# Kernel optimization log

Hardware: AMD Instinct MI355X
Metric: run time of the kernel (lower is better)

Reference implementation:

```python
import jax, jax.numpy as jnp
import numpy as np

B, IN, OUT, NC, S = 4096, 512, 512, 64, 1


def setup_inputs() -> dict:
    key = jax.random.key(0)
    k = jax.random.split(key, 5)
    x = jax.random.normal(k[0], (B, IN), dtype=jnp.float32)
    centers = jax.random.normal(k[1], (NC, IN), dtype=jnp.float32)
    log_sigma = jnp.zeros((NC,), dtype=jnp.float32)
    coeff_mean = jax.random.normal(k[2], (IN, OUT, NC), dtype=jnp.float32) * 0.05
    coeff_log_var = jnp.full((IN, OUT, NC), -5.0, dtype=jnp.float32)
    base_weight = jax.random.normal(k[3], (IN, OUT), dtype=jnp.float32) * 0.05
    eps = jax.random.normal(k[4], (S, IN, OUT, NC), dtype=jnp.float32)
    return {"x": x, "centers": centers, "log_sigma": log_sigma,
            "coeff_mean": coeff_mean, "coeff_log_var": coeff_log_var,
            "base_weight": base_weight, "eps": eps}


def reference(x, centers, log_sigma, coeff_mean, coeff_log_var, base_weight, eps):
    # RBF basis: (B, NC). Original repeats this along in_features, but the
    # einsum 'bin,ion->bo' with an i-constant basis equals rbf @ coeffs.sum(i).
    dist_sq = jnp.sum((x[:, None, :] - centers[None, :, :]) ** 2, axis=-1)  # (B, NC)
    sigma = jnp.exp(log_sigma)  # (NC,)
    rbf = jnp.exp(-dist_sq / (2.0 * sigma ** 2 + 1e-8))  # (B, NC)

    # Sampled variational coefficients, reparameterized.
    std = jnp.exp(0.5 * coeff_log_var)
    coeffs = coeff_mean + eps * std            # (S, IN, OUT, NC)
    c_sum = coeffs.sum(axis=1)                 # (S, OUT, NC): sum over in_features
    n_samples = eps.shape[0]
    rbf_out = jnp.einsum('bn,son->bo', rbf, c_sum) / n_samples  # mean over samples

    out = rbf_out + x @ base_weight

    # KL vs N(0, 1) prior (prior_scale = 1.0): log(var/prior_var) = coeff_log_var
    var = jnp.exp(coeff_log_var)
    kl = 0.5 * jnp.sum(var + coeff_mean ** 2 - 1.0 - coeff_log_var)
    return out, kl
```

## Files before the change

kernel.cpp:

```cpp
#include <hip/hip_runtime.h>
#include <hip/hip_bf16.h>

#define B_SZ  4096
#define IN_F  512
#define OUT_F 512
#define NC    64
#define PAIRS 32768
#define TOT   (IN_F * PAIRS)
#define KTOT  (IN_F + NC)
#define RCH   64

typedef __attribute__((ext_vector_type(8))) short bf16x8;
typedef __attribute__((ext_vector_type(4))) float f32x4;

static __device__ inline unsigned short f2bf(float f) {
    __hip_bfloat16 h = __float2bfloat16(f);
    return *(unsigned short*)&h;
}

__global__ __launch_bounds__(1024)
void k1_partial(const float* __restrict__ cm,
                const float* __restrict__ clv,
                const float* __restrict__ eps,
                float* __restrict__ part,
                float* __restrict__ klpart,
                int S) {
    int pb = blockIdx.x & 7;
    int rc = blockIdx.x >> 3;
    int p4 = pb * 4096 + threadIdx.x * 4;
    float Sf = (float)S;
    float4 s = {0.f, 0.f, 0.f, 0.f};
    float klp = 0.f;

#pragma unroll 4
    for (int ii = 0; ii < 8; ++ii) {
        size_t idx = (size_t)(rc * 8 + ii) * PAIRS + p4;
        float4 m  = *(const float4*)(cm  + idx);
        float4 lv = *(const float4*)(clv + idx);
        float4 es = *(const float4*)(eps + idx);
        for (int si = 1; si < S; ++si) {
            float4 e2 = *(const float4*)(eps + (size_t)si * TOT + idx);
            es.x += e2.x; es.y += e2.y; es.z += e2.z; es.w += e2.w;
        }
        float e1x = __expf(0.5f * lv.x);
        float e1y = __expf(0.5f * lv.y);
        float e1z = __expf(0.5f * lv.z);
        float e1w = __expf(0.5f * lv.w);
        s.x += Sf * m.x + es.x * e1x;
        s.y += Sf * m.y + es.y * e1y;
        s.z += Sf * m.z + es.z * e1z;
        s.w += Sf * m.w + es.w * e1w;
        klp += (e1x*e1x + m.x*m.x - 1.f - lv.x);
        klp += (e1y*e1y + m.y*m.y - 1.f - lv.y);
        klp += (e1z*e1z + m.z*m.z - 1.f - lv.z);
        klp += (e1w*e1w + m.w*m.w - 1.f - lv.w);
    }

    *(float4*)(part + (size_t)rc * PAIRS + p4) = s;

    for (int off = 32; off; off >>= 1)
        klp += __shfl_down(klp, off, 64);
    __shared__ float wsum[16];
    if ((threadIdx.x & 63) == 0) wsum[threadIdx.x >> 6] = klp;
    __syncthreads();
    if (threadIdx.x == 0) {
        float t = 0.f;
#pragma unroll
        for (int i = 0; i < 16; ++i) t += wsum[i];
        klpart[blockIdx.x] = t;
    }
}

__global__ __launch_bounds__(256)
void k_mid(const float* __restrict__ part,
           const float* __restrict__ klpart,
           const float* __restrict__ bw,
           unsigned short* __restrict__ wct,
           float* __restrict__ kl_out,
           float inv_S) {
    __shared__ float tile[64 * 68];
    __shared__ float wsum[4];
    int bid = blockIdx.x, t = threadIdx.x;

    if (bid < 128) {
        int p = bid * 256 + t;
        float a = 0.f;
#pragma unroll 8
        for (int r = 0; r < RCH; ++r)
            a += part[(size_t)r * PAIRS + p];
        int o = p >> 6, n = p & 63;
        wct[(size_t)o * KTOT + IN_F + n] = f2bf(a * inv_S);
    } else if (bid < 192) {
        int bb = bid - 128;
        int bi = bb >> 3, bj = bb & 7;
        int cq = t & 15, rq = t >> 4;
#pragma unroll
        for (int rr = 0; rr < 4; ++rr) {
            int row = rq * 4 + rr;
            float4 v = *(const float4*)(bw + (size_t)(bi * 64 + row) * OUT_F + bj * 64 + cq * 4);
            *(float4*)&tile[row * 68 + cq * 4] = v;
        }
        __syncthreads();
#pragma unroll
        for (int rr = 0; rr < 4; ++rr) {
            int orow = rq * 4 + rr;
            ushort4 w;
            w.x = f2bf(tile[(cq * 4 + 0) * 68 + orow]);
            w.y = f2bf(tile[(cq * 4 + 1) * 68 + orow]);
            w.z = f2bf(tile[(cq * 4 + 2) * 68 + orow]);
            w.w = f2bf(tile[(cq * 4 + 3) * 68 + orow]);
            *(ushort4*)(wct + (size_t)(bj * 64 + orow) * KTOT + bi * 64 + cq * 4) = w;
        }
    } else {
        float v = klpart[t] + klpart[t + 256];
        for (int off = 32; off; off >>= 1)
            v += __shfl_down(v, off, 64);
        if ((t & 63) == 0) wsum[t >> 6] = v;
        __syncthreads();
        if (t == 0)
            kl_out[0] = 0.5f * (wsum[0] + wsum[1] + wsum[2] + wsum[3]);
    }
}

__global__ __launch_bounds__(512)
void k2_rbf(const float* __restrict__ x,
            const float* __restrict__ centers,
            const float* __restrict__ log_sigma,
            unsigned short* __restrict__ rbf) {
    __shared__ float red[16][8][64];
    int t = threadIdx.x;
    int n = t & 63;
    int wu = __builtin_amdgcn_readfirstlane(t >> 6);
    int b0 = blockIdx.x * 16;

    float creg[64];
#pragma unroll
    for (int q = 0; q < 16; ++q) {
        float4 v = *(const float4*)(centers + (size_t)n * IN_F + wu * 64 + q * 4);
        creg[q * 4 + 0] = v.x; creg[q * 4 + 1] = v.y;
        creg[q * 4 + 2] = v.z; creg[q * 4 + 3] = v.w;
    }

    float dacc[16];
#pragma unroll
    for (int bi = 0; bi < 16; ++bi) {
        const float* xr = x + (size_t)(b0 + bi) * IN_F + wu * 64;
        float d0 = 0.f, d1 = 0.f, d2 = 0.f, d3 = 0.f;
#pragma unroll
        for (int j = 0; j < 64; j += 4) {
            float t0 = xr[j + 0] - creg[j + 0];
            float t1 = xr[j + 1] - creg[j + 1];
            float t2 = xr[j + 2] - creg[j + 2];
            float t3 = xr[j + 3] - creg[j + 3];
            d0 = fmaf(t0, t0, d0); d1 = fmaf(t1, t1, d1);
            d2 = fmaf(t2, t2, d2); d3 = fmaf(t3, t3, d3);
        }
        dacc[bi] = (d0 + d1) + (d2 + d3);
    }

#pragma unroll
    for (int bi = 0; bi < 16; ++bi)
        red[bi][wu][n] = dacc[bi];
    __syncthreads();

#pragma unroll
    for (int pass = 0; pass < 2; ++pass) {
        int idx = pass * 512 + t;
        int bi = idx >> 6, nn = idx & 63;
        float s = 0.f;
#pragma unroll
        for (int w = 0; w < 8; ++w) s += red[bi][w][nn];
        float sg  = __expf(log_sigma[nn]);
        float inv = 1.f / (2.f * sg * sg + 1e-8f);
        rbf[(size_t)(b0 + bi) * NC + nn] = f2bf(__expf(-s * inv));
    }
}

__global__ __launch_bounds__(256)
void k3_mfma(const float* __restrict__ x,
             const unsigned short* __restrict__ rbf,
             const unsigned short* __restrict__ wct,
             float* __restrict__ out) {
    __shared__ __align__(16) unsigned short As[64 * 40];
    __shared__ __align__(16) unsigned short Bs[64 * 40];
    int t = threadIdx.x;
    int bm = blockIdx.x >> 3, bn = blockIdx.x & 7;
    int b0 = bm * 64, o0 = bn * 64;
    int r = t >> 2, ks = t & 3;
    int lane = t & 63, wv = t >> 6;
    int fm = lane & 15, kg = lane >> 4;

    f32x4 acc[4] = {{0,0,0,0},{0,0,0,0},{0,0,0,0},{0,0,0,0}};
    const int soff = r * 40 + ks * 8;
    const int aoff = (wv * 16 + fm) * 40 + kg * 8;

    for (int it = 0; it < 16; ++it) {
        int k0 = it * 32;
        float4 xa = *(const float4*)(x + (size_t)(b0 + r) * IN_F + k0 + ks * 8);
        float4 xb = *(const float4*)(x + (size_t)(b0 + r) * IN_F + k0 + ks * 8 + 4);
        ushort4 w0 = *(const ushort4*)(wct + (size_t)(o0 + r) * KTOT + k0 + ks * 8);
        ushort4 w1 = *(const ushort4*)(wct + (size_t)(o0 + r) * KTOT + k0 + ks * 8 + 4);
        __syncthreads();
        ushort4 a0 = {f2bf(xa.x), f2bf(xa.y), f2bf(xa.z), f2bf(xa.w)};
        ushort4 a1 = {f2bf(xb.x), f2bf(xb.y), f2bf(xb.z), f2bf(xb.w)};
        *(ushort4*)&As[soff]     = a0;
        *(ushort4*)&As[soff + 4] = a1;
        *(ushort4*)&Bs[soff]     = w0;
        *(ushort4*)&Bs[soff + 4] = w1;
        __syncthreads();
        bf16x8 af = *(bf16x8*)&As[aoff];
#pragma unroll
        for (int nf = 0; nf < 4; ++nf) {
            bf16x8 bfr = *(bf16x8*)&Bs[(nf * 16 + fm) * 40 + kg * 8];
            acc[nf] = __builtin_amdgcn_mfma_f32_16x16x32_bf16(af, bfr, acc[nf], 0, 0, 0);
        }
    }

    for (int it = 0; it < 2; ++it) {
        int k0 = it * 32;
        ushort4 r0 = *(const ushort4*)(rbf + (size_t)(b0 + r) * NC + k0 + ks * 8);
        ushort4 r1 = *(const ushort4*)(rbf + (size_t)(b0 + r) * NC + k0 + ks * 8 + 4);
        ushort4 w0 = *(const ushort4*)(wct + (size_t)(o0 + r) * KTOT + IN_F + k0 + ks * 8);
        ushort4 w1 = *(const ushort4*)(wct + (size_t)(o0 + r) * KTOT + IN_F + k0 + ks * 8 + 4);
        __syncthreads();
        *(ushort4*)&As[soff]     = r0;
        *(ushort4*)&As[soff + 4] = r1;
        *(ushort4*)&Bs[soff]     = w0;
        *(ushort4*)&Bs[soff + 4] = w1;
        __syncthreads();
        bf16x8 af = *(bf16x8*)&As[aoff];
#pragma unroll
        for (int nf = 0; nf < 4; ++nf) {
            bf16x8 bfr = *(bf16x8*)&Bs[(nf * 16 + fm) * 40 + kg * 8];
            acc[nf] = __builtin_amdgcn_mfma_f32_16x16x32_bf16(af, bfr, acc[nf], 0, 0, 0);
        }
    }

#pragma unroll
    for (int nf = 0; nf < 4; ++nf)
#pragma unroll
        for (int rr = 0; rr < 4; ++rr)
            out[(size_t)(b0 + wv * 16 + kg * 4 + rr) * OUT_F + o0 + nf * 16 + fm] = acc[nf][rr];
}

extern "C" void kernel_launch(void* const* d_in, const int* in_sizes, int n_in,
                              void* d_out, int out_size, void* d_ws, size_t ws_size,
                              hipStream_t stream) {
    const float* x         = (const float*)d_in[0];
    const float* centers   = (const float*)d_in[1];
    const float* log_sigma = (const float*)d_in[2];
    const float* cm        = (const float*)d_in[3];
    const float* clv       = (const float*)d_in[4];
    const float* bw        = (const float*)d_in[5];
    const float* eps       = (const float*)d_in[6];

    float* out = (float*)d_out;
    float* kl  = out + (size_t)B_SZ * OUT_F;

    float* part   = (float*)d_ws;
    float* klpart = part + (size_t)RCH * PAIRS;
    unsigned short* wct = (unsigned short*)(klpart + 512);
    unsigned short* rbf = wct + (size_t)OUT_F * KTOT;

    int S = in_sizes[6] / TOT;

    k1_partial<<<512, 1024, 0, stream>>>(cm, clv, eps, part, klpart, S);
    k_mid<<<193, 256, 0, stream>>>(part, klpart, bw, wct, kl, 1.0f / (float)S);
    k2_rbf<<<B_SZ / 16, 512, 0, stream>>>(x, centers, log_sigma, rbf);
    k3_mfma<<<(B_SZ / 64) * (OUT_F / 64), 256, 0, stream>>>(x, rbf, wct, out);
}
```

Before: 264.8 us.

## Fuse RBF kernel into mid kernel and batch loads in partial reduction

```diff
diff --git a/kernel.cpp b/kernel.cpp
--- a/kernel.cpp
+++ b/kernel.cpp
@@ -18,92 +18,155 @@
     return *(unsigned short*)&h;
 }
 
-__global__ __launch_bounds__(1024)
+__global__ __launch_bounds__(512)
 void k1_partial(const float* __restrict__ cm,
                 const float* __restrict__ clv,
                 const float* __restrict__ eps,
                 float* __restrict__ part,
                 float* __restrict__ klpart,
                 int S) {
-    int pb = blockIdx.x & 7;
-    int rc = blockIdx.x >> 3;
-    int p4 = pb * 4096 + threadIdx.x * 4;
+    int pb = blockIdx.x & 15;
+    int rc = blockIdx.x >> 4;
+    int p4 = pb * 2048 + (threadIdx.x << 2);
+    size_t base = (size_t)(rc * 8) * PAIRS + p4;
     float Sf = (float)S;
+
+    float4 M[8], LV[8], ES[8];
+#pragma unroll
+    for (int ii = 0; ii < 8; ++ii)
+        M[ii] = *(const float4*)(cm + base + (size_t)ii * PAIRS);
+#pragma unroll
+    for (int ii = 0; ii < 8; ++ii)
+        LV[ii] = *(const float4*)(clv + base + (size_t)ii * PAIRS);
+#pragma unroll
+    for (int ii = 0; ii < 8; ++ii)
+        ES[ii] = *(const float4*)(eps + base + (size_t)ii * PAIRS);
+    for (int si = 1; si < S; ++si)
+#pragma unroll
+        for (int ii = 0; ii < 8; ++ii) {
+            float4 e = *(const float4*)(eps + (size_t)si * TOT + base + (size_t)ii * PAIRS);
+            ES[ii].x += e.x; ES[ii].y += e.y; ES[ii].z += e.z; ES[ii].w += e.w;
+        }
+
     float4 s = {0.f, 0.f, 0.f, 0.f};
     float klp = 0.f;
-
-#pragma unroll 4
+#pragma unroll
     for (int ii = 0; ii < 8; ++ii) {
-        size_t idx = (size_t)(rc * 8 + ii) * PAIRS + p4;
-        float4 m  = *(const float4*)(cm  + idx);
-        float4 lv = *(const float4*)(clv + idx);
-        float4 es = *(const float4*)(eps + idx);
-        for (int si = 1; si < S; ++si) {
-            float4 e2 = *(const float4*)(eps + (size_t)si * TOT + idx);
-            es.x += e2.x; es.y += e2.y; es.z += e2.z; es.w += e2.w;
-        }
-        float e1x = __expf(0.5f * lv.x);
-        float e1y = __expf(0.5f * lv.y);
-        float e1z = __expf(0.5f * lv.z);
-        float e1w = __expf(0.5f * lv.w);
-        s.x += Sf * m.x + es.x * e1x;
-        s.y += Sf * m.y + es.y * e1y;
-        s.z += Sf * m.z + es.z * e1z;
-        s.w += Sf * m.w + es.w * e1w;
-        klp += (e1x*e1x + m.x*m.x - 1.f - lv.x);
-        klp += (e1y*e1y + m.y*m.y - 1.f - lv.y);
-        klp += (e1z*e1z + m.z*m.z - 1.f - lv.z);
-        klp += (e1w*e1w + m.w*m.w - 1.f - lv.w);
+        float e1x = __expf(0.5f * LV[ii].x);
+        float e1y = __expf(0.5f * LV[ii].y);
+        float e1z = __expf(0.5f * LV[ii].z);
+        float e1w = __expf(0.5f * LV[ii].w);
+        s.x += Sf * M[ii].x + ES[ii].x * e1x;
+        s.y += Sf * M[ii].y + ES[ii].y * e1y;
+        s.z += Sf * M[ii].z + ES[ii].z * e1z;
+        s.w += Sf * M[ii].w + ES[ii].w * e1w;
+        klp += (e1x*e1x + M[ii].x*M[ii].x - 1.f - LV[ii].x);
+        klp += (e1y*e1y + M[ii].y*M[ii].y - 1.f - LV[ii].y);
+        klp += (e1z*e1z + M[ii].z*M[ii].z - 1.f - LV[ii].z);
+        klp += (e1w*e1w + M[ii].w*M[ii].w - 1.f - LV[ii].w);
     }
 
     *(float4*)(part + (size_t)rc * PAIRS + p4) = s;
 
     for (int off = 32; off; off >>= 1)
         klp += __shfl_down(klp, off, 64);
-    __shared__ float wsum[16];
+    __shared__ float wsum[8];
     if ((threadIdx.x & 63) == 0) wsum[threadIdx.x >> 6] = klp;
     __syncthreads();
     if (threadIdx.x == 0) {
         float t = 0.f;
 #pragma unroll
-        for (int i = 0; i < 16; ++i) t += wsum[i];
+        for (int i = 0; i < 8; ++i) t += wsum[i];
         klpart[blockIdx.x] = t;
     }
 }
 
-__global__ __launch_bounds__(256)
-void k_mid(const float* __restrict__ part,
+__global__ __launch_bounds__(512)
+void k_mid(const float* __restrict__ x,
+           const float* __restrict__ centers,
+           const float* __restrict__ log_sigma,
+           const float* __restrict__ part,
            const float* __restrict__ klpart,
            const float* __restrict__ bw,
+           unsigned short* __restrict__ rbf,
            unsigned short* __restrict__ wct,
            float* __restrict__ kl_out,
            float inv_S) {
-    __shared__ float tile[64 * 68];
-    __shared__ float wsum[4];
+    __shared__ float shbuf[16 * 8 * 64];
     int bid = blockIdx.x, t = threadIdx.x;
 
-    if (bid < 128) {
-        int p = bid * 256 + t;
-        float a = 0.f;
-#pragma unroll 8
-        for (int r = 0; r < RCH; ++r)
-            a += part[(size_t)r * PAIRS + p];
+    if (bid < 256) {
+        float (*red)[8][64] = (float (*)[8][64])shbuf;
+        int n = t & 63;
+        int wu = __builtin_amdgcn_readfirstlane(t >> 6);
+        int b0 = bid * 16;
+
+        float creg[64];
+#pragma unroll
+        for (int q = 0; q < 16; ++q) {
+            float4 v = *(const float4*)(centers + (size_t)n * IN_F + wu * 64 + q * 4);
+            creg[q * 4 + 0] = v.x; creg[q * 4 + 1] = v.y;
+            creg[q * 4 + 2] = v.z; creg[q * 4 + 3] = v.w;
+        }
+
+        float dacc[16];
+#pragma unroll
+        for (int bi = 0; bi < 16; ++bi) {
+            const float* xr = x + (size_t)(b0 + bi) * IN_F + wu * 64;
+            float d0 = 0.f, d1 = 0.f, d2 = 0.f, d3 = 0.f;
+#pragma unroll
+            for (int j = 0; j < 64; j += 4) {
+                float t0 = xr[j + 0] - creg[j + 0];
+                float t1 = xr[j + 1] - creg[j + 1];
+                float t2 = xr[j + 2] - creg[j + 2];
+                float t3 = xr[j + 3] - creg[j + 3];
+                d0 = fmaf(t0, t0, d0); d1 = fmaf(t1, t1, d1);
+                d2 = fmaf(t2, t2, d2); d3 = fmaf(t3, t3, d3);
+            }
+            dacc[bi] = (d0 + d1) + (d2 + d3);
+        }
+#pragma unroll
+        for (int bi = 0; bi < 16; ++bi)
+            red[bi][wu][n] = dacc[bi];
+        __syncthreads();
+#pragma unroll
+        for (int pass = 0; pass < 2; ++pass) {
+            int idx = pass * 512 + t;
+            int bi = idx >> 6, nn = idx & 63;
+            float ssum = 0.f;
+#pragma unroll
+            for (int w = 0; w < 8; ++w) ssum += red[bi][w][nn];
+            float sg  = __expf(log_sigma[nn]);
+            float inv = 1.f / (2.f * sg * sg + 1e-8f);
+            rbf[(size_t)(b0 + bi) * NC + nn] = f2bf(__expf(-ssum * inv));
+        }
+    } else if (bid < 320) {
+        int p = (bid - 256) * 512 + t;
+        float a0 = 0.f, a1 = 0.f, a2 = 0.f, a3 = 0.f;
+#pragma unroll
+        for (int r = 0; r < RCH; r += 4) {
+            a0 += part[(size_t)(r + 0) * PAIRS + p];
+            a1 += part[(size_t)(r + 1) * PAIRS + p];
+            a2 += part[(size_t)(r + 2) * PAIRS + p];
+            a3 += part[(size_t)(r + 3) * PAIRS + p];
+        }
         int o = p >> 6, n = p & 63;
-        wct[(size_t)o * KTOT + IN_F + n] = f2bf(a * inv_S);
-    } else if (bid < 192) {
-        int bb = bid - 128;
+        wct[(size_t)o * KTOT + IN_F + n] = f2bf(((a0 + a1) + (a2 + a3)) * inv_S);
+    } else if (bid < 384) {
+        float* tile = shbuf;
+        int bb = bid - 320;
         int bi = bb >> 3, bj = bb & 7;
         int cq = t & 15, rq = t >> 4;
 #pragma unroll
-        for (int rr = 0; rr < 4; ++rr) {
-            int row = rq * 4 + rr;
+        for (int rr = 0; rr < 2; ++rr) {
+            int row = rq * 2 + rr;
             float4 v = *(const float4*)(bw + (size_t)(bi * 64 + row) * OUT_F + bj * 64 + cq * 4);
             *(float4*)&tile[row * 68 + cq * 4] = v;
         }
         __syncthreads();
 #pragma unroll
-        for (int rr = 0; rr < 4; ++rr) {
-            int orow = rq * 4 + rr;
+        for (int rr = 0; rr < 2; ++rr) {
+            int orow = rq * 2 + rr;
             ushort4 w;
             w.x = f2bf(tile[(cq * 4 + 0) * 68 + orow]);
             w.y = f2bf(tile[(cq * 4 + 1) * 68 + orow]);
@@ -112,67 +175,18 @@
             *(ushort4*)(wct + (size_t)(bj * 64 + orow) * KTOT + bi * 64 + cq * 4) = w;
         }
     } else {
-        float v = klpart[t] + klpart[t + 256];
+        float v = klpart[t] + klpart[t + 512];
         for (int off = 32; off; off >>= 1)
             v += __shfl_down(v, off, 64);
+        float* wsum = shbuf;
         if ((t & 63) == 0) wsum[t >> 6] = v;
         __syncthreads();
-        if (t == 0)
-            kl_out[0] = 0.5f * (wsum[0] + wsum[1] + wsum[2] + wsum[3]);
-    }
-}
-
-__global__ __launch_bounds__(512)
-void k2_rbf(const float* __restrict__ x,
-            const float* __restrict__ centers,
-            const float* __restrict__ log_sigma,
-            unsigned short* __restrict__ rbf) {
-    __shared__ float red[16][8][64];
-    int t = threadIdx.x;
-    int n = t & 63;
-    int wu = __builtin_amdgcn_readfirstlane(t >> 6);
-    int b0 = blockIdx.x * 16;
-
-    float creg[64];
-#pragma unroll
-    for (int q = 0; q < 16; ++q) {
-        float4 v = *(const float4*)(centers + (size_t)n * IN_F + wu * 64 + q * 4);
-        creg[q * 4 + 0] = v.x; creg[q * 4 + 1] = v.y;
-        creg[q * 4 + 2] = v.z; creg[q * 4 + 3] = v.w;
-    }
-
-    float dacc[16];
-#pragma unroll
-    for (int bi = 0; bi < 16; ++bi) {
-        const float* xr = x + (size_t)(b0 + bi) * IN_F + wu * 64;
-        float d0 = 0.f, d1 = 0.f, d2 = 0.f, d3 = 0.f;
-#pragma unroll
-        for (int j = 0; j < 64; j += 4) {
-            float t0 = xr[j + 0] - creg[j + 0];
-            float t1 = xr[j + 1] - creg[j + 1];
-            float t2 = xr[j + 2] - creg[j + 2];
-            float t3 = xr[j + 3] - creg[j + 3];
-            d0 = fmaf(t0, t0, d0); d1 = fmaf(t1, t1, d1);
-            d2 = fmaf(t2, t2, d2); d3 = fmaf(t3, t3, d3);
-        }
-        dacc[bi] = (d0 + d1) + (d2 + d3);
-    }
-
-#pragma unroll
-    for (int bi = 0; bi < 16; ++bi)
-        red[bi][wu][n] = dacc[bi];
-    __syncthreads();
-
-#pragma unroll
-    for (int pass = 0; pass < 2; ++pass) {
-        int idx = pass * 512 + t;
-        int bi = idx >> 6, nn = idx & 63;
-        float s = 0.f;
-#pragma unroll
-        for (int w = 0; w < 8; ++w) s += red[bi][w][nn];
-        float sg  = __expf(log_sigma[nn]);
-        float inv = 1.f / (2.f * sg * sg + 1e-8f);
-        rbf[(size_t)(b0 + bi) * NC + nn] = f2bf(__expf(-s * inv));
+        if (t == 0) {
+            float s = 0.f;
+#pragma unroll
+            for (int i = 0; i < 8; ++i) s += wsum[i];
+            kl_out[0] = 0.5f * s;
+        }
     }
 }
 
@@ -259,13 +273,13 @@
 
     float* part   = (float*)d_ws;
     float* klpart = part + (size_t)RCH * PAIRS;
-    unsigned short* wct = (unsigned short*)(klpart + 512);
+    unsigned short* wct = (unsigned short*)(klpart + 1024);
     unsigned short* rbf = wct + (size_t)OUT_F * KTOT;
 
     int S = in_sizes[6] / TOT;
 
-    k1_partial<<<512, 1024, 0, stream>>>(cm, clv, eps, part, klpart, S);
-    k_mid<<<193, 256, 0, stream>>>(part, klpart, bw, wct, kl, 1.0f / (float)S);
-    k2_rbf<<<B_SZ / 16, 512, 0, stream>>>(x, centers, log_sigma, rbf);
+    k1_partial<<<1024, 512, 0, stream>>>(cm, clv, eps, part, klpart, S);
+    k_mid<<<385, 512, 0, stream>>>(x, centers, log_sigma, part, klpart, bw,
+                                   rbf, wct, kl, 1.0f / (float)S);
     k3_mfma<<<(B_SZ / 64) * (OUT_F / 64), 256, 0, stream>>>(x, rbf, wct, out);
 }
```

Result: no change. 259.9 us (-1.8%).
